# Optimization experiments

Hardware: AMD Instinct MI355X
Metric: run time of the kernel (lower is better)

## Reference

```python
import jax, jax.numpy as jnp
import numpy as np

N_NODES = 50000
N_EDGES = 800000
D = 128
AVG_D_LOG = 2.833  # log(avg_degree + 1)
EPS = 1e-5


def setup_inputs() -> dict:
    key = jax.random.key(0)
    ks = jax.random.split(key, 8)
    h = jax.random.normal(ks[0], (N_NODES, D), dtype=jnp.float32)
    e = jax.random.normal(ks[1], (N_EDGES, D), dtype=jnp.float32)
    snorm_n = jax.random.uniform(ks[2], (N_NODES, 1), dtype=jnp.float32)
    src = jax.random.randint(ks[3], (N_EDGES,), 0, N_NODES)
    dst = jax.random.randint(ks[4], (N_EDGES,), 0, N_NODES)
    W_pre = jax.random.normal(ks[5], (3 * D, D), dtype=jnp.float32) * 0.05
    b_pre = jnp.zeros((D,), dtype=jnp.float32)
    W_post = jax.random.normal(ks[6], (13 * D, D), dtype=jnp.float32) * 0.05
    b_post = jnp.zeros((D,), dtype=jnp.float32)
    return {"h": h, "e": e, "snorm_n": snorm_n, "src": src, "dst": dst,
            "W_pre": W_pre, "b_pre": b_pre, "W_post": W_post, "b_post": b_post}


def _pna_forward(h, e, snorm_n, src, dst, W_pre, b_pre, W_post, b_post):
    N = h.shape[0]
    # pretrans_edges: gather endpoint features + edge features, single Linear (pretrans_layers=1)
    z2 = jnp.concatenate([h[src], h[dst], e], axis=1)           # [E, 3D]
    m = z2 @ W_pre + b_pre                                        # [E, D] per-edge message

    # reduce: multi-aggregator mailbox reduce over dst (ragged neighborhoods)
    deg = jax.ops.segment_sum(jnp.ones((m.shape[0],), m.dtype), dst, num_segments=N)  # [N]
    deg_safe = jnp.maximum(deg, 1.0)[:, None]
    s = jax.ops.segment_sum(m, dst, num_segments=N)
    s2 = jax.ops.segment_sum(m * m, dst, num_segments=N)
    mean = s / deg_safe
    var = jax.nn.relu(s2 / deg_safe - mean * mean)
    std = jnp.sqrt(var + EPS)
    mx = jax.ops.segment_max(m, dst, num_segments=N)
    mn = jax.ops.segment_min(m, dst, num_segments=N)
    has = (deg > 0)[:, None]
    mx = jnp.where(has, mx, 0.0)
    mn = jnp.where(has, mn, 0.0)
    agg = jnp.concatenate([mean, mx, mn, std], axis=1)            # [N, 4D]

    # scalers: identity, amplification, attenuation
    log_d = jnp.log(deg[:, None] + 1.0)
    log_d_safe = jnp.log(deg_safe + 1.0)
    amp = agg * (log_d / AVG_D_LOG)
    att = agg * (AVG_D_LOG / log_d_safe)
    scaled = jnp.concatenate([agg, amp, att], axis=1)             # [N, 12D]
    scaled = jnp.where(has, scaled, 0.0)                          # DGL zero-fills zero-degree nodes

    # posttrans: cat original h, single Linear (posttrans_layers=1), then graph_norm
    h_cat = jnp.concatenate([h, scaled], axis=1)                  # [N, 13D]
    out = h_cat @ W_post + b_post                                 # [N, D]
    out = out * snorm_n                                           # graph_norm; dropout p=0 is identity
    return out


def reference(h, e, snorm_n, src, dst, W_pre, b_pre, W_post, b_post):
    return _pna_forward(h, e, snorm_n, src, dst, W_pre, b_pre, W_post, b_post)
```

## Files before the change

### kernel.cpp

```cpp
#include <hip/hip_runtime.h>
#include <math.h>

#define NNODES 50000
#define NEDGES 800000
#define AVGDLOG 2.833f
#define EPSF 1e-5f
#define TPB_E 8
#define NSCAN 49

typedef __attribute__((ext_vector_type(8))) short short8;
typedef __attribute__((ext_vector_type(4))) float f32x4;

__device__ __forceinline__ unsigned f2bf(float x) {
    unsigned u = __float_as_uint(x);
    return (u + 0x7FFFu + ((u >> 16) & 1u)) >> 16;
}
__device__ __forceinline__ float bf2f(unsigned lo16) {
    return __uint_as_float(lo16 << 16);
}
__device__ __forceinline__ void up8(uint4 v, float* f) {
    f[0] = bf2f(v.x & 0xffffu); f[1] = bf2f(v.x >> 16);
    f[2] = bf2f(v.y & 0xffffu); f[3] = bf2f(v.y >> 16);
    f[4] = bf2f(v.z & 0xffffu); f[5] = bf2f(v.z >> 16);
    f[6] = bf2f(v.w & 0xffffu); f[7] = bf2f(v.w >> 16);
}
__device__ __forceinline__ uint4 pk8(const float* f) {
    uint4 v;
    v.x = f2bf(f[0]) | (f2bf(f[1]) << 16);
    v.y = f2bf(f[2]) | (f2bf(f[3]) << 16);
    v.z = f2bf(f[4]) | (f2bf(f[5]) << 16);
    v.w = f2bf(f[6]) | (f2bf(f[7]) << 16);
    return v;
}

__global__ void k_zero(unsigned* __restrict__ deg) {
    int i = blockIdx.x * 256 + threadIdx.x;
    if (i < NNODES) deg[i] = 0u;
}
__global__ void k_count(const int* __restrict__ dst, unsigned* __restrict__ deg) {
    int i = blockIdx.x * 256 + threadIdx.x;
    if (i < NEDGES) atomicAdd(&deg[dst[i]], 1u);
}
__global__ void k_scanA(const unsigned* __restrict__ deg, int* __restrict__ bsum) {
    __shared__ int wsum[4];
    const int t = threadIdx.x, b = blockIdx.x;
    int i = b * 1024 + t * 4;
    int s = 0;
    if (i + 4 <= NNODES) {
        int4 v = *(const int4*)(deg + i);
        s = v.x + v.y + v.z + v.w;
    } else {
        for (int k = 0; k < 4; ++k) if (i + k < NNODES) s += (int)deg[i + k];
    }
#pragma unroll
    for (int off = 1; off < 64; off <<= 1) s += __shfl_xor(s, off);
    if ((t & 63) == 0) wsum[t >> 6] = s;
    __syncthreads();
    if (t == 0) bsum[b] = wsum[0] + wsum[1] + wsum[2] + wsum[3];
}
__global__ void k_scanB(const int* __restrict__ bsum, int* __restrict__ boff,
                        int* __restrict__ basep) {
    if (threadIdx.x == 0) {
        int run = 0;
        for (int b = 0; b < NSCAN; ++b) { boff[b] = run; run += bsum[b]; }
        basep[NNODES] = run;
    }
}
__global__ void k_scanC(const unsigned* __restrict__ deg, const int* __restrict__ boff,
                        int* __restrict__ basep, int* __restrict__ cursor) {
    __shared__ int ps[256];
    const int t = threadIdx.x, b = blockIdx.x;
    int i = b * 1024 + t * 4;
    int v0 = 0, v1 = 0, v2 = 0, v3 = 0;
    if (i + 4 <= NNODES) {
        int4 v = *(const int4*)(deg + i);
        v0 = v.x; v1 = v.y; v2 = v.z; v3 = v.w;
    } else {
        if (i < NNODES) v0 = (int)deg[i];
        if (i + 1 < NNODES) v1 = (int)deg[i + 1];
        if (i + 2 < NNODES) v2 = (int)deg[i + 2];
        if (i + 3 < NNODES) v3 = (int)deg[i + 3];
    }
    int ts = v0 + v1 + v2 + v3;
    ps[t] = ts;
    __syncthreads();
    for (int off = 1; off < 256; off <<= 1) {
        int x = (t >= off) ? ps[t - off] : 0;
        __syncthreads();
        ps[t] += x;
        __syncthreads();
    }
    int excl = ps[t] - ts + boff[b];
    if (i < NNODES) { basep[i] = excl; cursor[i] = excl; }
    if (i + 1 < NNODES) { basep[i + 1] = excl + v0; cursor[i + 1] = excl + v0; }
    if (i + 2 < NNODES) { basep[i + 2] = excl + v0 + v1; cursor[i + 2] = excl + v0 + v1; }
    if (i + 3 < NNODES) { basep[i + 3] = excl + v0 + v1 + v2; cursor[i + 3] = excl + v0 + v1 + v2; }
}
__global__ void k_scatter(const int* __restrict__ dst, int* __restrict__ cursor,
                          int* __restrict__ slotArr) {
    int i = blockIdx.x * 256 + threadIdx.x;
    if (i < NEDGES) {
        int d = dst[i];
        slotArr[i] = atomicAdd(&cursor[d], 1);
    }
}

__global__ void k_convW(const float* __restrict__ Wpre, const float* __restrict__ Wpost,
                        unsigned short* __restrict__ W3t, unsigned short* __restrict__ W12t,
                        unsigned short* __restrict__ Bhat) {
    int i = blockIdx.x * 256 + threadIdx.x;
    if (i < 128 * 128) {
        int n = i & 127, k = i >> 7;
        W3t[n * 128 + k] = (unsigned short)f2bf(Wpre[(256 + k) * 128 + n]);
    }
    if (i < 256 * 128) {
        int n = i >> 7, k = i & 127;
        float v = (n < 128) ? Wpre[k * 128 + n] : Wpre[(128 + k) * 128 + (n - 128)];
        W12t[n * 128 + k] = (unsigned short)f2bf(v);
    }
    if (i < 640 * 384) {
        int kc = i / (384 * 32);
        int rem = i % (384 * 32);
        int n = rem >> 5, kk = rem & 31;
        int k = kc * 32 + kk, c = n & 127, g = n >> 7;
        float v;
        if (g == 0) v = Wpost[k * 128 + c];
        else if (g == 1) v = (k < 128) ? 0.f : Wpost[(512 + k) * 128 + c];
        else v = (k < 128) ? 0.f : Wpost[(1024 + k) * 128 + c];
        Bhat[i] = (unsigned short)f2bf(v);
    }
}

__global__ __launch_bounds__(256) void k_p12(const float* __restrict__ h,
                                             const unsigned short* __restrict__ W12t,
                                             unsigned short* __restrict__ P1,
                                             unsigned short* __restrict__ P2,
                                             unsigned short* __restrict__ Abuf) {
    __shared__ __align__(16) unsigned short As[64 * 128];
    __shared__ __align__(16) unsigned short Bs[256 * 128];
    const int t = threadIdx.x;
    const size_t row0 = (size_t)blockIdx.x * 64;
#pragma unroll
    for (int j = 0; j < 16; ++j) {
        int idx = t + 256 * j;
        int n = idx >> 4, q = idx & 15;
        uint4 wv = *(const uint4*)(W12t + n * 128 + q * 8);
        *(uint4*)((char*)Bs + n * 256 + ((q * 16) ^ ((n & 7) << 4))) = wv;
    }
#pragma unroll
    for (int j = 0; j < 8; ++j) {
        int idx = t + 256 * j;
        int r = idx >> 5, q = idx & 31;
        size_t row = row0 + r;
        uint2 p = {0u, 0u};
        if (row < NNODES) {
            float4 z = ((const float4*)h)[row * 32 + q];
            p.x = f2bf(z.x) | (f2bf(z.y) << 16);
            p.y = f2bf(z.z) | (f2bf(z.w) << 16);
            *(uint2*)(Abuf + row * 640 + q * 4) = p;
        }
        *(uint2*)((char*)As + r * 256 + ((q * 8) ^ ((r & 7) << 4))) = p;
    }
    __syncthreads();
    const int w = t >> 6, lane = t & 63, lrow = lane & 15, lkb = lane >> 4;
    f32x4 acc[16];
#pragma unroll
    for (int i = 0; i < 16; ++i) acc[i] = (f32x4){0.f, 0.f, 0.f, 0.f};
    const char* Abase = (const char*)As + (w * 16 + lrow) * 256;
    const unsigned aswz = (unsigned)(((w * 16 + lrow) & 7) << 4);
#pragma unroll
    for (int kk = 0; kk < 4; ++kk) {
        int kbyte = (kk * 32 + lkb * 8) * 2;
        short8 af = *(const short8*)(Abase + (kbyte ^ aswz));
#pragma unroll
        for (int nt = 0; nt < 16; ++nt) {
            int n = nt * 16 + lrow;
            short8 bf = *(const short8*)((const char*)Bs + n * 256 + (kbyte ^ ((n & 7) << 4)));
            acc[nt] = __builtin_amdgcn_mfma_f32_16x16x32_bf16(af, bf, acc[nt], 0, 0, 0);
        }
    }
#pragma unroll
    for (int half = 0; half < 2; ++half) {
        __syncthreads();
#pragma unroll
        for (int nt = 0; nt < 8; ++nt) {
            int c = nt * 16 + lrow;
#pragma unroll
            for (int i = 0; i < 4; ++i) {
                int lr = w * 16 + lkb * 4 + i;
                *(unsigned short*)((char*)As + lr * 256 + ((c * 2) ^ ((lr & 7) << 4))) =
                    (unsigned short)f2bf(acc[half * 8 + nt][i]);
            }
        }
        __syncthreads();
        unsigned short* dstP = half ? P2 : P1;
#pragma unroll
        for (int j = 0; j < 4; ++j) {
            int idx = t + 256 * j;
            int r = idx >> 4, q = idx & 15;
            size_t row = row0 + r;
            if (row < NNODES) {
                uint4 v = *(const uint4*)((const char*)As + r * 256 + ((q * 16) ^ ((r & 7) << 4)));
                *(uint4*)(dstP + row * 128 + q * 8) = v;
            }
        }
    }
}

__global__ __launch_bounds__(256) void k_gemm_e(const float* __restrict__ e,
                                                const int* __restrict__ src,
                                                const int* __restrict__ slotArr,
                                                const unsigned short* __restrict__ W3t,
                                                const float* __restrict__ bpre,
                                                const unsigned short* __restrict__ P1,
                                                unsigned short* __restrict__ G) {
    __shared__ __align__(16) unsigned short Bs[128 * 128];
    __shared__ __align__(16) unsigned short As[64 * 128];
    __shared__ int Ssl[TPB_E * 64];
    __shared__ int Ssr[TPB_E * 64];
    const int t = threadIdx.x;
    const int tile0 = blockIdx.x * TPB_E;
    const int ntiles = min(TPB_E, 12500 - tile0);

    for (int j = t; j < ntiles * 64; j += 256) {
        int row = tile0 * 64 + j;
        Ssl[j] = slotArr[row];
        Ssr[j] = src[row];
    }

    const int q = t & 31, r5 = t >> 5;
    float4 rbuf[2][8];
    auto loadE = [&](int ti, float4* ra) {
        const float4* ep = (const float4*)e + (size_t)(tile0 + ti) * 2048;
#pragma unroll
        for (int j = 0; j < 8; ++j)
            ra[j] = ep[(r5 + 8 * j) * 32 + q];
    };
    auto storeA = [&](const float4* ra) {
#pragma unroll
        for (int j = 0; j < 8; ++j) {
            int r = r5 + 8 * j;
            uint2 pv;
            pv.x = f2bf(ra[j].x) | (f2bf(ra[j].y) << 16);
            pv.y = f2bf(ra[j].z) | (f2bf(ra[j].w) << 16);
            *(uint2*)((char*)As + r * 256 + ((q * 8) ^ ((r & 7) << 4))) = pv;
        }
    };

    loadE(0, rbuf[0]);
#pragma unroll
    for (int j = 0; j < 8; ++j) {
        int idx = t + 256 * j;
        int n = idx >> 4, qq = idx & 15;
        uint4 wv = *(const uint4*)(W3t + n * 128 + qq * 8);
        *(uint4*)((char*)Bs + n * 256 + ((qq * 16) ^ ((n & 7) << 4))) = wv;
    }
    if (ntiles > 1) loadE(1, rbuf[1]);

    const int w = t >> 6, lane = t & 63, lrow = lane & 15, lkb = lane >> 4;
    float bpf[8];
#pragma unroll
    for (int nt = 0; nt < 8; ++nt) bpf[nt] = bpre[nt * 16 + lrow];

    for (int ti = 0; ti < ntiles; ++ti) {
        storeA(rbuf[ti & 1]);
        if (ti + 2 < ntiles) loadE(ti + 2, rbuf[ti & 1]);
        __syncthreads();
        f32x4 acc[8];
#pragma unroll
        for (int i = 0; i < 8; ++i) acc[i] = (f32x4){0.f, 0.f, 0.f, 0.f};
        const char* Ab = (const char*)As + (w * 16 + lrow) * 256;
        const unsigned aswz = (unsigned)(((w * 16 + lrow) & 7) << 4);
#pragma unroll
        for (int kk = 0; kk < 4; ++kk) {
            int kbyte = (kk * 32 + lkb * 8) * 2;
            short8 af = *(const short8*)(Ab + (kbyte ^ aswz));
#pragma unroll
            for (int nt = 0; nt < 8; ++nt) {
                int n = nt * 16 + lrow;
                short8 bf = *(const short8*)((const char*)Bs + n * 256 + (kbyte ^ ((n & 7) << 4)));
                acc[nt] = __builtin_amdgcn_mfma_f32_16x16x32_bf16(af, bf, acc[nt], 0, 0, 0);
            }
        }
        __syncthreads();
#pragma unroll
        for (int nt = 0; nt < 8; ++nt) {
            int cc = nt * 16 + lrow;
#pragma unroll
            for (int i = 0; i < 4; ++i) {
                int lr = w * 16 + lkb * 4 + i;
                *(unsigned short*)((char*)As + lr * 256 + ((cc * 2) ^ ((lr & 7) << 4))) =
                    (unsigned short)f2bf(acc[nt][i] + bpf[nt]);
            }
        }
        __syncthreads();
#pragma unroll
        for (int j = 0; j < 4; ++j) {
            int idx = t + 256 * j;
            int r = idx >> 4, qq = idx & 15;
            uint4 v = *(const uint4*)((const char*)As + r * 256 + ((qq * 16) ^ ((r & 7) << 4)));
            uint4 pv = *(const uint4*)(P1 + (size_t)Ssr[ti * 64 + r] * 128 + qq * 8);
            float gf[8], pf[8];
            up8(v, gf); up8(pv, pf);
#pragma unroll
            for (int k = 0; k < 8; ++k) gf[k] += pf[k];
            *(uint4*)(G + (size_t)Ssl[ti * 64 + r] * 128 + qq * 8) = pk8(gf);
        }
        __syncthreads();
    }
}

__global__ __launch_bounds__(256) void k_reduce(const unsigned short* __restrict__ G,
                                                const unsigned short* __restrict__ P2,
                                                const int* __restrict__ basep,
                                                unsigned short* __restrict__ Abuf) {
    const int t = threadIdx.x;
    const int n = blockIdx.x * 4 + (t >> 6);
    const int lane = t & 63, lq = lane >> 4, lc = lane & 15;
    int b0 = basep[n], b1 = basep[n + 1];
    int dg = b1 - b0;
    float s[8], q2[8], mx[8], mn[8];
#pragma unroll
    for (int j = 0; j < 8; ++j) { s[j] = 0.f; q2[j] = 0.f; mx[j] = -3.4e38f; mn[j] = 3.4e38f; }
    for (int sl = b0 + lq; sl < b1; sl += 4) {
        float gf[8];
        up8(*(const uint4*)(G + (size_t)sl * 128 + lc * 8), gf);
#pragma unroll
        for (int j = 0; j < 8; ++j) {
            float m = gf[j];
            s[j] += m; q2[j] = fmaf(m, m, q2[j]);
            mx[j] = fmaxf(mx[j], m); mn[j] = fminf(mn[j], m);
        }
    }
#pragma unroll
    for (int off = 16; off <= 32; off <<= 1) {
#pragma unroll
        for (int j = 0; j < 8; ++j) {
            s[j] += __shfl_xor(s[j], off);
            q2[j] += __shfl_xor(q2[j], off);
            mx[j] = fmaxf(mx[j], __shfl_xor(mx[j], off));
            mn[j] = fminf(mn[j], __shfl_xor(mn[j], off));
        }
    }
    if (lane < 16) {
        float mean[8], sd[8], X[8], N[8];
        if (dg > 0) {
            float ds = (float)dg;
            float p2f[8];
            up8(*(const uint4*)(P2 + (size_t)n * 128 + lc * 8), p2f);
#pragma unroll
            for (int j = 0; j < 8; ++j) {
                float mg = s[j] / ds;
                float v = fmaxf(q2[j] / ds - mg * mg, 0.f);
                sd[j] = sqrtf(v + EPSF);
                mean[j] = mg + p2f[j];
                X[j] = mx[j] + p2f[j];
                N[j] = mn[j] + p2f[j];
            }
        } else {
#pragma unroll
            for (int j = 0; j < 8; ++j) { mean[j] = 0.f; sd[j] = 0.f; X[j] = 0.f; N[j] = 0.f; }
        }
        unsigned short* row = Abuf + (size_t)n * 640 + 128 + lc * 8;
        *(uint4*)(row) = pk8(mean);
        *(uint4*)(row + 128) = pk8(X);
        *(uint4*)(row + 256) = pk8(N);
        *(uint4*)(row + 384) = pk8(sd);
    }
}

__global__ __launch_bounds__(512) void k_gemm_post(const unsigned short* __restrict__ Abuf,
                                                   const unsigned short* __restrict__ Bhat,
                                                   const float* __restrict__ bpost,
                                                   const float* __restrict__ snorm,
                                                   const int* __restrict__ basep,
                                                   float* __restrict__ out) {
    __shared__ __align__(16) unsigned short As[2][128 * 32];
    __shared__ __align__(16) unsigned short Bs[2][384 * 32];
    __shared__ float sAmp[128], sAtt[128], sSn[128], sBp[128];
    const int t = threadIdx.x;
    const size_t row0 = (size_t)blockIdx.x * 128;
    if (t < 128) {
        size_t nn = row0 + t;
        float a = 0.f, b = 0.f, sn = 0.f;
        if (nn < NNODES) {
            int dgi = basep[nn + 1] - basep[nn];
            a = logf((float)dgi + 1.f) * (1.f / AVGDLOG);
            b = AVGDLOG / logf(fmaxf((float)dgi, 1.f) + 1.f);
            sn = snorm[nn];
        }
        sAmp[t] = a; sAtt[t] = b; sSn[t] = sn; sBp[t] = bpost[t];
    }
    const int arow = t >> 2, ak4 = t & 3;
    auto loadA = [&](int kc, uint4& ra) {
        ra = (uint4){0u, 0u, 0u, 0u};
        if (row0 + arow < NNODES)
            ra = *(const uint4*)(Abuf + (row0 + arow) * 640 + kc * 32 + ak4 * 8);
    };
    auto loadB = [&](int kc, uint4* rb) {
#pragma unroll
        for (int j = 0; j < 3; ++j) {
            int idx = t + 512 * j;
            int n = idx >> 2, k4 = idx & 3;
            rb[j] = *(const uint4*)(Bhat + ((size_t)kc * 384 + n) * 32 + k4 * 8);
        }
    };
    auto storeLDS = [&](int buf, const uint4& ra, const uint4* rb) {
        *(uint4*)((char*)As[buf] + arow * 64 + ((ak4 * 16) ^ ((arow & 3) << 4))) = ra;
#pragma unroll
        for (int j = 0; j < 3; ++j) {
            int idx = t + 512 * j;
            int n = idx >> 2, k4 = idx & 3;
            *(uint4*)((char*)Bs[buf] + n * 64 + ((k4 * 16) ^ ((n & 3) << 4))) = rb[j];
        }
    };
    const int w = t >> 6, wm = w & 1, wn = w >> 1;
    const int lane = t & 63, lrow = lane & 15, lkb = lane >> 4;
    f32x4 acc[4][6];
#pragma unroll
    for (int a = 0; a < 4; ++a)
#pragma unroll
        for (int b = 0; b < 6; ++b) acc[a][b] = (f32x4){0.f, 0.f, 0.f, 0.f};

    uint4 ra, rb[3];
    loadA(0, ra); loadB(0, rb);
    storeLDS(0, ra, rb);
    int cur = 0;
    for (int kc = 0; kc < 20; ++kc) {
        if (kc < 19) { loadA(kc + 1, ra); loadB(kc + 1, rb); }
        __syncthreads();
        short8 af[4];
#pragma unroll
        for (int mi = 0; mi < 4; ++mi) {
            int r = wm * 64 + mi * 16 + lrow;
            af[mi] = *(const short8*)((const char*)As[cur] + r * 64 + ((lkb * 16) ^ ((r & 3) << 4)));
        }
        short8 bfv[6];
#pragma unroll
        for (int g = 0; g < 3; ++g)
#pragma unroll
            for (int j = 0; j < 2; ++j) {
                int nn = g * 128 + wn * 32 + j * 16 + lrow;
                bfv[g * 2 + j] = *(const short8*)((const char*)Bs[cur] + nn * 64 + ((lkb * 16) ^ ((nn & 3) << 4)));
            }
#pragma unroll
        for (int mi = 0; mi < 4; ++mi)
#pragma unroll
            for (int f = 0; f < 6; ++f)
                acc[mi][f] = __builtin_amdgcn_mfma_f32_16x16x32_bf16(af[mi], bfv[f], acc[mi][f], 0, 0, 0);
        if (kc < 19) storeLDS(cur ^ 1, ra, rb);
        cur ^= 1;
    }
#pragma unroll
    for (int mi = 0; mi < 4; ++mi)
#pragma unroll
        for (int j = 0; j < 2; ++j)
#pragma unroll
            for (int i = 0; i < 4; ++i) {
                int r = wm * 64 + mi * 16 + lkb * 4 + i;
                size_t grow = row0 + r;
                if (grow < NNODES) {
                    int c = wn * 32 + j * 16 + lrow;
                    float v = acc[mi][j][i] + sAmp[r] * acc[mi][2 + j][i] + sAtt[r] * acc[mi][4 + j][i] + sBp[c];
                    out[grow * 128 + c] = v * sSn[r];
                }
            }
}

extern "C" void kernel_launch(void* const* d_in, const int* in_sizes, int n_in,
                              void* d_out, int out_size, void* d_ws, size_t ws_size,
                              hipStream_t stream) {
    const float* h = (const float*)d_in[0];
    const float* e = (const float*)d_in[1];
    const float* snorm = (const float*)d_in[2];
    const int* src = (const int*)d_in[3];
    const int* dst = (const int*)d_in[4];
    const float* Wpre = (const float*)d_in[5];
    const float* bpre = (const float*)d_in[6];
    const float* Wpost = (const float*)d_in[7];
    const float* bpost = (const float*)d_in[8];
    float* out = (float*)d_out;

    char* p = (char*)d_ws;
    auto alloc = [&](size_t bytes) { char* r = p; p += (bytes + 255) & ~(size_t)255; return r; };
    unsigned short* P1 = (unsigned short*)alloc((size_t)NNODES * 128 * 2);
    unsigned short* P2 = (unsigned short*)alloc((size_t)NNODES * 128 * 2);
    unsigned short* Abuf = (unsigned short*)alloc((size_t)NNODES * 640 * 2);
    unsigned short* G = (unsigned short*)alloc((size_t)NEDGES * 128 * 2);
    unsigned short* W3t = (unsigned short*)alloc(128 * 128 * 2);
    unsigned short* W12t = (unsigned short*)alloc(256 * 128 * 2);
    unsigned short* Bhat = (unsigned short*)alloc((size_t)640 * 384 * 2);
    unsigned* deg = (unsigned*)alloc((size_t)NNODES * 4);
    int* basep = (int*)alloc((size_t)(NNODES + 1) * 4);
    int* cursor = (int*)alloc((size_t)NNODES * 4);
    int* slotArr = (int*)alloc((size_t)NEDGES * 4);
    int* bsum = (int*)alloc((size_t)NSCAN * 4);
    int* boff = (int*)alloc((size_t)NSCAN * 4);

    k_zero<<<(NNODES + 255) / 256, 256, 0, stream>>>(deg);
    k_count<<<(NEDGES + 255) / 256, 256, 0, stream>>>(dst, deg);
    k_scanA<<<NSCAN, 256, 0, stream>>>(deg, bsum);
    k_scanB<<<1, 64, 0, stream>>>(bsum, boff, basep);
    k_scanC<<<NSCAN, 256, 0, stream>>>(deg, boff, basep, cursor);
    k_scatter<<<(NEDGES + 255) / 256, 256, 0, stream>>>(dst, cursor, slotArr);
    k_convW<<<(640 * 384 + 255) / 256, 256, 0, stream>>>(Wpre, Wpost, W3t, W12t, Bhat);
    k_p12<<<(NNODES + 63) / 64, 256, 0, stream>>>(h, W12t, P1, P2, Abuf);
    k_gemm_e<<<(12500 + TPB_E - 1) / TPB_E, 256, 0, stream>>>(e, src, slotArr, W3t, bpre, P1, G);
    k_reduce<<<NNODES / 4, 256, 0, stream>>>(G, P2, basep, Abuf);
    k_gemm_post<<<(NNODES + 127) / 128, 512, 0, stream>>>(Abuf, Bhat, bpost, snorm, basep, out);
}
```

Baseline: 559.8 us.

## Load edge features directly into MFMA A-fragments, dropping LDS staging and prefetch

The edge-message GEMM kernel now reads each lane's fp32 slice of e straight from global memory, converts it to bf16 and feeds it to the MFMA as the A operand. The LDS write of the A tile, its read-back and one barrier per tile are removed. The cost is that the double-buffered register prefetch of the next tiles is gone, so global load latency is no longer hidden behind compute. Each lane also now reads two float4 per k-step with a 512-byte row stride, which may coalesce less well than the old row-contiguous pattern.

```diff
diff --git a/kernel.cpp b/kernel.cpp
--- a/kernel.cpp
+++ b/kernel.cpp
@@ -227,27 +227,6 @@
         Ssl[j] = slotArr[row];
         Ssr[j] = src[row];
     }
-
-    const int q = t & 31, r5 = t >> 5;
-    float4 rbuf[2][8];
-    auto loadE = [&](int ti, float4* ra) {
-        const float4* ep = (const float4*)e + (size_t)(tile0 + ti) * 2048;
-#pragma unroll
-        for (int j = 0; j < 8; ++j)
-            ra[j] = ep[(r5 + 8 * j) * 32 + q];
-    };
-    auto storeA = [&](const float4* ra) {
-#pragma unroll
-        for (int j = 0; j < 8; ++j) {
-            int r = r5 + 8 * j;
-            uint2 pv;
-            pv.x = f2bf(ra[j].x) | (f2bf(ra[j].y) << 16);
-            pv.y = f2bf(ra[j].z) | (f2bf(ra[j].w) << 16);
-            *(uint2*)((char*)As + r * 256 + ((q * 8) ^ ((r & 7) << 4))) = pv;
-        }
-    };
-
-    loadE(0, rbuf[0]);
 #pragma unroll
     for (int j = 0; j < 8; ++j) {
         int idx = t + 256 * j;
@@ -255,31 +234,40 @@
         uint4 wv = *(const uint4*)(W3t + n * 128 + qq * 8);
         *(uint4*)((char*)Bs + n * 256 + ((qq * 16) ^ ((n & 7) << 4))) = wv;
     }
-    if (ntiles > 1) loadE(1, rbuf[1]);
 
     const int w = t >> 6, lane = t & 63, lrow = lane & 15, lkb = lane >> 4;
     float bpf[8];
 #pragma unroll
     for (int nt = 0; nt < 8; ++nt) bpf[nt] = bpre[nt * 16 + lrow];
+    const float* ebase = e + (size_t)(tile0 * 64 + w * 16 + lrow) * 128 + lkb * 8;
+
+    __syncthreads();
 
     for (int ti = 0; ti < ntiles; ++ti) {
-        storeA(rbuf[ti & 1]);
-        if (ti + 2 < ntiles) loadE(ti + 2, rbuf[ti & 1]);
-        __syncthreads();
+        const float* ep = ebase + (size_t)ti * 64 * 128;
+        short8 af[4];
+#pragma unroll
+        for (int kk = 0; kk < 4; ++kk) {
+            float4 a0 = *(const float4*)(ep + kk * 32);
+            float4 a1 = *(const float4*)(ep + kk * 32 + 4);
+            union { short8 s; unsigned u[4]; } cv;
+            cv.u[0] = f2bf(a0.x) | (f2bf(a0.y) << 16);
+            cv.u[1] = f2bf(a0.z) | (f2bf(a0.w) << 16);
+            cv.u[2] = f2bf(a1.x) | (f2bf(a1.y) << 16);
+            cv.u[3] = f2bf(a1.z) | (f2bf(a1.w) << 16);
+            af[kk] = cv.s;
+        }
         f32x4 acc[8];
 #pragma unroll
         for (int i = 0; i < 8; ++i) acc[i] = (f32x4){0.f, 0.f, 0.f, 0.f};
-        const char* Ab = (const char*)As + (w * 16 + lrow) * 256;
-        const unsigned aswz = (unsigned)(((w * 16 + lrow) & 7) << 4);
 #pragma unroll
         for (int kk = 0; kk < 4; ++kk) {
             int kbyte = (kk * 32 + lkb * 8) * 2;
-            short8 af = *(const short8*)(Ab + (kbyte ^ aswz));
 #pragma unroll
             for (int nt = 0; nt < 8; ++nt) {
                 int n = nt * 16 + lrow;
                 short8 bf = *(const short8*)((const char*)Bs + n * 256 + (kbyte ^ ((n & 7) << 4)));
-                acc[nt] = __builtin_amdgcn_mfma_f32_16x16x32_bf16(af, bf, acc[nt], 0, 0, 0);
+                acc[nt] = __builtin_amdgcn_mfma_f32_16x16x32_bf16(af[kk], bf, acc[nt], 0, 0, 0);
             }
         }
         __syncthreads();
@@ -306,7 +294,6 @@
             for (int k = 0; k < 8; ++k) gf[k] += pf[k];
             *(uint4*)(G + (size_t)Ssl[ti * 64 + r] * 128 + qq * 8) = pk8(gf);
         }
-        __syncthreads();
     }
 }
 
```

Measured after the change: 484.8 us. -13.4%, faster.

## Make edge GEMM tiles wave-private to drop block-wide barriers

Applied to the files above, without the earlier changes.

Each wave now loads, converts and stores its own 16 rows of the edge-feature tile into shared memory, runs the MFMA on those rows, writes the result back, and scatters the same rows. The tile no longer has to be shared across the block, so the four __syncthreads per tile are removed. The register double-buffered prefetch of e is dropped, so global-load latency is no longer hidden by the earlier prefetch and must be covered by other waves. Correctness relies on wave-level ordering of LDS accesses within each wave's private rows.

```diff
diff --git a/kernel.cpp b/kernel.cpp
--- a/kernel.cpp
+++ b/kernel.cpp
@@ -227,27 +227,6 @@
         Ssl[j] = slotArr[row];
         Ssr[j] = src[row];
     }
-
-    const int q = t & 31, r5 = t >> 5;
-    float4 rbuf[2][8];
-    auto loadE = [&](int ti, float4* ra) {
-        const float4* ep = (const float4*)e + (size_t)(tile0 + ti) * 2048;
-#pragma unroll
-        for (int j = 0; j < 8; ++j)
-            ra[j] = ep[(r5 + 8 * j) * 32 + q];
-    };
-    auto storeA = [&](const float4* ra) {
-#pragma unroll
-        for (int j = 0; j < 8; ++j) {
-            int r = r5 + 8 * j;
-            uint2 pv;
-            pv.x = f2bf(ra[j].x) | (f2bf(ra[j].y) << 16);
-            pv.y = f2bf(ra[j].z) | (f2bf(ra[j].w) << 16);
-            *(uint2*)((char*)As + r * 256 + ((q * 8) ^ ((r & 7) << 4))) = pv;
-        }
-    };
-
-    loadE(0, rbuf[0]);
 #pragma unroll
     for (int j = 0; j < 8; ++j) {
         int idx = t + 256 * j;
@@ -255,22 +234,33 @@
         uint4 wv = *(const uint4*)(W3t + n * 128 + qq * 8);
         *(uint4*)((char*)Bs + n * 256 + ((qq * 16) ^ ((n & 7) << 4))) = wv;
     }
-    if (ntiles > 1) loadE(1, rbuf[1]);
+    __syncthreads();
 
     const int w = t >> 6, lane = t & 63, lrow = lane & 15, lkb = lane >> 4;
+    const int q5 = lane & 31, rh = lane >> 5;
     float bpf[8];
 #pragma unroll
     for (int nt = 0; nt < 8; ++nt) bpf[nt] = bpre[nt * 16 + lrow];
 
     for (int ti = 0; ti < ntiles; ++ti) {
-        storeA(rbuf[ti & 1]);
-        if (ti + 2 < ntiles) loadE(ti + 2, rbuf[ti & 1]);
-        __syncthreads();
+        const float4* ep = (const float4*)e + ((size_t)(tile0 + ti) * 64 + w * 16) * 32;
+        float4 ra[8];
+#pragma unroll
+        for (int j = 0; j < 8; ++j)
+            ra[j] = ep[(j * 2 + rh) * 32 + q5];
+#pragma unroll
+        for (int j = 0; j < 8; ++j) {
+            int r = w * 16 + j * 2 + rh;
+            uint2 pv;
+            pv.x = f2bf(ra[j].x) | (f2bf(ra[j].y) << 16);
+            pv.y = f2bf(ra[j].z) | (f2bf(ra[j].w) << 16);
+            *(uint2*)((char*)As + r * 256 + ((q5 * 8) ^ ((r & 7) << 4))) = pv;
+        }
         f32x4 acc[8];
 #pragma unroll
         for (int i = 0; i < 8; ++i) acc[i] = (f32x4){0.f, 0.f, 0.f, 0.f};
         const char* Ab = (const char*)As + (w * 16 + lrow) * 256;
-        const unsigned aswz = (unsigned)(((w * 16 + lrow) & 7) << 4);
+        const unsigned aswz = (unsigned)((lrow & 7) << 4);
 #pragma unroll
         for (int kk = 0; kk < 4; ++kk) {
             int kbyte = (kk * 32 + lkb * 8) * 2;
@@ -282,7 +272,6 @@
                 acc[nt] = __builtin_amdgcn_mfma_f32_16x16x32_bf16(af, bf, acc[nt], 0, 0, 0);
             }
         }
-        __syncthreads();
 #pragma unroll
         for (int nt = 0; nt < 8; ++nt) {
             int cc = nt * 16 + lrow;
@@ -293,20 +282,20 @@
                     (unsigned short)f2bf(acc[nt][i] + bpf[nt]);
             }
         }
-        __syncthreads();
 #pragma unroll
         for (int j = 0; j < 4; ++j) {
-            int idx = t + 256 * j;
-            int r = idx >> 4, qq = idx & 15;
-            uint4 v = *(const uint4*)((const char*)As + r * 256 + ((qq * 16) ^ ((r & 7) << 4)));
-            uint4 pv = *(const uint4*)(P1 + (size_t)Ssr[ti * 64 + r] * 128 + qq * 8);
+            int idx = lane + 64 * j;
+            int rl = idx >> 4, qq = idx & 15;
+            int r = w * 16 + rl;
+            uint4 v = *(const uint4*)((const char*)As + r * 256 + ((qq * 16) ^ ((rl & 7) << 4)));
+            int meta = ti * 64 + r;
+            uint4 pv = *(const uint4*)(P1 + (size_t)Ssr[meta] * 128 + qq * 8);
             float gf[8], pf[8];
             up8(v, gf); up8(pv, pf);
 #pragma unroll
             for (int k = 0; k < 8; ++k) gf[k] += pf[k];
-            *(uint4*)(G + (size_t)Ssl[ti * 64 + r] * 128 + qq * 8) = pk8(gf);
-        }
-        __syncthreads();
+            *(uint4*)(G + (size_t)Ssl[meta] * 128 + qq * 8) = pk8(gf);
+        }
     }
 }
 
```

New measurement: 567.5 us. No clear change (+1.4%).
